# Optimization experiments

Measured on AMD Instinct MI355X. Metric: run time of the kernel, lower is better.

## Reference

```python
import jax, jax.numpy as jnp
import numpy as np

NUM_IN, NUM_OUT, K, G = 128, 128, 3, 5
SIZE = NUM_IN * NUM_OUT
BATCH = 512


def _extend_grid(grid, k):
    # pykan-style extension: add k uniformly spaced knots on each side
    h = (grid[:, -1:] - grid[:, :1]) / (grid.shape[1] - 1)
    for _ in range(k):
        grid = jnp.concatenate([grid[:, :1] - h, grid, grid[:, -1:] + h], axis=1)
    return grid


def _b_batch(x, grid, k):
    # Cox-de Boor recursion. x: (size, batch), grid: (size, G+1)
    g = _extend_grid(grid, k)[:, :, None]          # (size, G+1+2k, 1)
    xe = x[:, None, :]                             # (size, 1, batch)
    B = ((xe >= g[:, :-1]) & (xe < g[:, 1:])).astype(x.dtype)  # degree-0: (size, G+2k, batch)
    for p in range(1, k + 1):
        B = (xe - g[:, :-(p + 1)]) / (g[:, p:-1] - g[:, :-(p + 1)]) * B[:, :-1] \
          + (g[:, p + 1:] - xe) / (g[:, p + 1:] - g[:, 1:-p]) * B[:, 1:]
    return B                                       # (size, G+k, batch)


def _coef_to_curve(x_eval, grid, coef, k):
    return jnp.einsum('sj,sjb->sb', coef, _b_batch(x_eval, grid, k))


def setup_inputs():
    key = jax.random.key(0)
    k1, k2 = jax.random.split(key)
    x = jax.random.normal(k1, (BATCH, NUM_IN), dtype=jnp.float32)
    knots = jnp.tile(jnp.linspace(-1.0, 1.0, G + 1, dtype=jnp.float32)[None, :], (SIZE, 1))
    coef = jax.random.normal(k2, (SIZE, G + K), dtype=jnp.float32) * 0.1
    scale_b = jnp.ones((SIZE, 1), dtype=jnp.float32)
    scale_spline = jnp.ones((SIZE, 1), dtype=jnp.float32)
    mask = jnp.ones((SIZE,), dtype=jnp.float32)
    return {"x": x, "scale_b": scale_b, "scale_spline": scale_spline,
            "coef": coef, "mask": mask, "knots": knots}


def reference(x, scale_b, scale_spline, coef, mask, knots):
    batch = x.shape[0]
    # x.unsqueeze(1).repeat(1, num_out, 1).reshape(-1, size).T -> (size, batch)
    pre_acts = jnp.broadcast_to(x[:, None, :], (batch, NUM_OUT, NUM_IN)).reshape(batch, SIZE).T
    post_splines = _coef_to_curve(pre_acts, knots, coef, K) * mask[:, None]
    post_acts = scale_b * jax.nn.silu(pre_acts) + scale_spline * post_splines
    # reshape(num_in, num_out, batch).permute(2,0,1).sum(dim=1) as in the original
    y = post_acts.reshape(NUM_IN, NUM_OUT, batch).transpose(2, 0, 1).sum(axis=1)
    return (y, pre_acts.T, post_splines.T, post_acts.T)
```

## Files before the change

### kernel.cpp

```cpp
#include <hip/hip_runtime.h>
#include <math.h>


#define N_IN   128
#define SIZEK  16384
#define BATCH  512

#define TB 4
#define CO 4

__global__ __launch_bounds__(256) void kan_fwd(
    const float* __restrict__ x,
    const float* __restrict__ scale_b,
    const float* __restrict__ scale_spline,
    const float* __restrict__ coef,
    const float* __restrict__ mask,
    const float* __restrict__ knots,
    float* __restrict__ y,
    float* __restrict__ pre_out,
    float* __restrict__ spl_out,
    float* __restrict__ post_out)
{
    const int g  = blockIdx.x * blockDim.x + threadIdx.x;
    const int i  = g & 127;
    const int r  = g >> 7;
    const int oc = r & 31;
    const int bg = r >> 5;
    const int o0 = oc << 2;
    const int b0 = bg << 2;

    float xv[TB], sil[TB], ysum[TB];
#pragma unroll
    for (int t = 0; t < TB; ++t) {
        const float xx = x[(b0 + t) * N_IN + i];
        xv[t]   = xx;
        sil[t]  = xx / (1.0f + __expf(-xx));
        ysum[t] = 0.0f;
    }

    float e0v[CO], ihv[CO], mkv[CO], sbv[CO], ssv[CO];
    float4 cA[CO], cB[CO];
#pragma unroll
    for (int oo = 0; oo < CO; ++oo) {
        const int s = ((o0 + oo) << 7) | i;
        const float k0 = knots[s * 6];
        const float k5 = knots[s * 6 + 5];
        const float h  = (k5 - k0) * 0.2f;
        ihv[oo] = 1.0f / h;
        e0v[oo] = k0 - 3.0f * h;
        mkv[oo] = mask[s];
        sbv[oo] = scale_b[s];
        ssv[oo] = scale_spline[s];
        const float4* c4 = (const float4*)(coef + (size_t)s * 8);
        cA[oo] = c4[0];
        cB[oo] = c4[1];
    }

#pragma unroll
    for (int oo = 0; oo < CO; ++oo) {
        const int s = ((o0 + oo) << 7) | i;
        const float e0   = e0v[oo];
        const float invh = ihv[oo];
        const float mk   = mkv[oo];
        const float sb   = sbv[oo];
        const float ss   = ssv[oo];
        const float c0 = cA[oo].x, c1 = cA[oo].y, c2 = cA[oo].z, c3 = cA[oo].w;
        const float c4 = cB[oo].x, c5 = cB[oo].y, c6 = cB[oo].z, c7 = cB[oo].w;

#pragma unroll
        for (int t = 0; t < TB; ++t) {
            const float u  = (xv[t] - e0) * invh;
            const float mf = floorf(u);
            const int   m  = (int)mf;
            const float tt = u - mf;
            const bool inr = (m >= 0) && (m <= 10);

            const float t2  = tt * tt;
            const float t3  = t2 * tt;
            const float omt = 1.0f - tt;
            float w[4];
            w[0] = omt * omt * omt * (1.0f / 6.0f);
            w[1] = (3.0f * t3 - 6.0f * t2 + 4.0f) * (1.0f / 6.0f);
            w[2] = (-3.0f * t3 + 3.0f * t2 + 3.0f * tt + 1.0f) * (1.0f / 6.0f);
            w[3] = t3 * (1.0f / 6.0f);

            const int jlo = m - 3;
            float spline = 0.0f;
#pragma unroll
            for (int rr = 0; rr < 4; ++rr) {
                const int j  = jlo + rr;
                const int jc = min(max(j, 0), 7);
                const float s01   = (jc & 1) ? c1 : c0;
                const float s23   = (jc & 1) ? c3 : c2;
                const float s45   = (jc & 1) ? c5 : c4;
                const float s67   = (jc & 1) ? c7 : c6;
                const float s0123 = (jc & 2) ? s23 : s01;
                const float s4567 = (jc & 2) ? s67 : s45;
                const float c     = (jc & 4) ? s4567 : s0123;
                const float wv = (inr && j >= 0 && j <= 7) ? w[rr] : 0.0f;
                spline = fmaf(c, wv, spline);
            }

            const float splm = spline * mk;
            const float post = fmaf(sb, sil[t], ss * splm);

            const size_t idx = (size_t)(b0 + t) * SIZEK + (size_t)s;
            __builtin_nontemporal_store(xv[t], &pre_out[idx]);
            __builtin_nontemporal_store(splm, &spl_out[idx]);
            __builtin_nontemporal_store(post, &post_out[idx]);
            ysum[t] += post;
        }
    }

#pragma unroll
    for (int t = 0; t < TB; ++t)
        atomicAdd(&y[(b0 + t) * N_IN + i], ysum[t]);
}

extern "C" void kernel_launch(void* const* d_in, const int* in_sizes, int n_in,
                              void* d_out, int out_size, void* d_ws, size_t ws_size,
                              hipStream_t stream) {
    const float* x            = (const float*)d_in[0];
    const float* scale_b      = (const float*)d_in[1];
    const float* scale_spline = (const float*)d_in[2];
    const float* coef         = (const float*)d_in[3];
    const float* mask         = (const float*)d_in[4];
    const float* knots        = (const float*)d_in[5];

    float* out  = (float*)d_out;
    float* y    = out;
    float* pre  = y + 512 * 128;
    float* spl  = pre + (size_t)512 * 16384;
    float* post = spl + (size_t)512 * 16384;

    (void)hipMemsetAsync(y, 0, 512 * 128 * sizeof(float), stream);

    dim3 grid(2048), block(256);
    kan_fwd<<<grid, block, 0, stream>>>(x, scale_b, scale_spline, coef, mask,
                                        knots, y, pre, spl, post);
}
```

Baseline: 127.2 us.

## Remap threads to one batch row per block and reduce y in shared memory

Each block now handles a single batch row and 32 input indices. Its 8 thread groups each cover 16 outputs, and the per-output partial sums are combined in shared memory and written straight to y. This removes the global atomics and the separate memset launch. In exchange, each thread no longer reuses the per-edge coefficients, knots and scales across several batch rows, so parameter loads per output rise about fourfold. Each 64-lane wavefront's stores are also split across two output rows.

```diff
diff --git a/kernel.cpp b/kernel.cpp
--- a/kernel.cpp
+++ b/kernel.cpp
@@ -4,10 +4,6 @@
 
 #define N_IN   128
 #define SIZEK  16384
-#define BATCH  512
-
-#define TB 4
-#define CO 4
 
 __global__ __launch_bounds__(256) void kan_fwd(
     const float* __restrict__ x,
@@ -21,55 +17,48 @@
     float* __restrict__ spl_out,
     float* __restrict__ post_out)
 {
-    const int g  = blockIdx.x * blockDim.x + threadIdx.x;
-    const int i  = g & 127;
-    const int r  = g >> 7;
-    const int oc = r & 31;
-    const int bg = r >> 5;
-    const int o0 = oc << 2;
-    const int b0 = bg << 2;
+    const int tid = threadIdx.x;
+    const int di  = tid & 31;
+    const int oct = tid >> 5;
+    const int ig  = blockIdx.x & 3;
+    const int b   = blockIdx.x >> 2;
+    const int i   = (ig << 5) | di;
 
-    float xv[TB], sil[TB], ysum[TB];
+    const float xx  = x[b * N_IN + i];
+    const float sil = xx / (1.0f + __expf(-xx));
+    float ysum = 0.0f;
+
+#pragma unroll 1
+    for (int oc4 = 0; oc4 < 4; ++oc4) {
+        const int o0 = (oct << 4) | (oc4 << 2);
+
+        float e0v[4], ihv[4], mkv[4], sbv[4], ssv[4];
+        float4 cAv[4], cBv[4];
 #pragma unroll
-    for (int t = 0; t < TB; ++t) {
-        const float xx = x[(b0 + t) * N_IN + i];
-        xv[t]   = xx;
-        sil[t]  = xx / (1.0f + __expf(-xx));
-        ysum[t] = 0.0f;
-    }
-
-    float e0v[CO], ihv[CO], mkv[CO], sbv[CO], ssv[CO];
-    float4 cA[CO], cB[CO];
-#pragma unroll
-    for (int oo = 0; oo < CO; ++oo) {
-        const int s = ((o0 + oo) << 7) | i;
-        const float k0 = knots[s * 6];
-        const float k5 = knots[s * 6 + 5];
-        const float h  = (k5 - k0) * 0.2f;
-        ihv[oo] = 1.0f / h;
-        e0v[oo] = k0 - 3.0f * h;
-        mkv[oo] = mask[s];
-        sbv[oo] = scale_b[s];
-        ssv[oo] = scale_spline[s];
-        const float4* c4 = (const float4*)(coef + (size_t)s * 8);
-        cA[oo] = c4[0];
-        cB[oo] = c4[1];
-    }
+        for (int oo = 0; oo < 4; ++oo) {
+            const int s = ((o0 + oo) << 7) | i;
+            const float k0 = knots[s * 6];
+            const float k5 = knots[s * 6 + 5];
+            const float h  = (k5 - k0) * 0.2f;
+            ihv[oo] = 1.0f / h;
+            e0v[oo] = k0 - 3.0f * h;
+            mkv[oo] = mask[s];
+            sbv[oo] = scale_b[s];
+            ssv[oo] = scale_spline[s];
+            const float4* c4 = (const float4*)(coef + (size_t)s * 8);
+            cAv[oo] = c4[0];
+            cBv[oo] = c4[1];
+        }
 
 #pragma unroll
-    for (int oo = 0; oo < CO; ++oo) {
-        const int s = ((o0 + oo) << 7) | i;
-        const float e0   = e0v[oo];
-        const float invh = ihv[oo];
-        const float mk   = mkv[oo];
-        const float sb   = sbv[oo];
-        const float ss   = ssv[oo];
-        const float c0 = cA[oo].x, c1 = cA[oo].y, c2 = cA[oo].z, c3 = cA[oo].w;
-        const float c4 = cB[oo].x, c5 = cB[oo].y, c6 = cB[oo].z, c7 = cB[oo].w;
+        for (int oo = 0; oo < 4; ++oo) {
+            const int s = ((o0 + oo) << 7) | i;
+            const float e0   = e0v[oo];
+            const float invh = ihv[oo];
+            const float c0 = cAv[oo].x, c1 = cAv[oo].y, c2 = cAv[oo].z, c3 = cAv[oo].w;
+            const float c4 = cBv[oo].x, c5 = cBv[oo].y, c6 = cBv[oo].z, c7 = cBv[oo].w;
 
-#pragma unroll
-        for (int t = 0; t < TB; ++t) {
-            const float u  = (xv[t] - e0) * invh;
+            const float u  = (xx - e0) * invh;
             const float mf = floorf(u);
             const int   m  = (int)mf;
             const float tt = u - mf;
@@ -101,20 +90,27 @@
                 spline = fmaf(c, wv, spline);
             }
 
-            const float splm = spline * mk;
-            const float post = fmaf(sb, sil[t], ss * splm);
+            const float splm = spline * mkv[oo];
+            const float post = fmaf(sbv[oo], sil, ssv[oo] * splm);
 
-            const size_t idx = (size_t)(b0 + t) * SIZEK + (size_t)s;
-            __builtin_nontemporal_store(xv[t], &pre_out[idx]);
+            const size_t idx = (size_t)b * SIZEK + (size_t)s;
+            __builtin_nontemporal_store(xx,   &pre_out[idx]);
             __builtin_nontemporal_store(splm, &spl_out[idx]);
             __builtin_nontemporal_store(post, &post_out[idx]);
-            ysum[t] += post;
+            ysum += post;
         }
     }
 
+    __shared__ float red[8][33];
+    red[oct][di] = ysum;
+    __syncthreads();
+    if (tid < 32) {
+        float a = 0.0f;
 #pragma unroll
-    for (int t = 0; t < TB; ++t)
-        atomicAdd(&y[(b0 + t) * N_IN + i], ysum[t]);
+        for (int d = 0; d < 8; ++d)
+            a += red[d][tid];
+        y[b * N_IN + (ig << 5) + tid] = a;
+    }
 }
 
 extern "C" void kernel_launch(void* const* d_in, const int* in_sizes, int n_in,
@@ -133,8 +129,6 @@
     float* spl  = pre + (size_t)512 * 16384;
     float* post = spl + (size_t)512 * 16384;
 
-    (void)hipMemsetAsync(y, 0, 512 * 128 * sizeof(float), stream);
-
     dim3 grid(2048), block(256);
     kan_fwd<<<grid, block, 0, stream>>>(x, scale_b, scale_spline, coef, mask,
                                         knots, y, pre, spl, post);
```

New measurement: 144.5 us. +13.6%, slower.
